# Optimization experiments

Measured on AMD Instinct MI355X. Metric: run time of the kernel, lower is better.

The kernel has to match this reference:

```python
import jax, jax.numpy as jnp
import numpy as np


def setup_inputs() -> dict:
    key = jax.random.key(0)
    # D must equal N for the elementwise Multiply([inputs, attn]) to broadcast.
    B, N = 16, 1024
    x = jax.random.normal(key, (B, N, N), dtype=jnp.float32)
    return {"x": x}


def reference(x) -> jnp.ndarray:
    # scores[b,i,j] = <x[b,i,:], x[b,j,:]>  -> [B, N, N]
    scores = jnp.einsum("bid,bjd->bij", x, x)
    attn = jax.nn.softmax(scores, axis=-1)
    # NOTE: elementwise multiply (not a weighted sum) — faithful to the source.
    return x * attn
```

## Files before the change

kernel.cpp:

```cpp
#include <hip/hip_runtime.h>
#include <hip/hip_bf16.h>

#define BATCH   16
#define NN      1024
#define ROWS    64
#define NWAVES  8
#define NTHR    512
#define KSTEP   32
#define NCT     8
#define MT      4

typedef __attribute__((ext_vector_type(8))) short short8;
typedef __attribute__((ext_vector_type(4))) float f32x4;

static __device__ __forceinline__ unsigned short cvt_bf16(float f) {
    unsigned int u = __builtin_bit_cast(unsigned int, f);
    u += 0x7fffu + ((u >> 16) & 1u);
    return (unsigned short)(u >> 16);
}

static __device__ __forceinline__ short8 cvt8(float4 u0, float4 u1) {
    short8 r;
    r[0] = (short)cvt_bf16(u0.x); r[1] = (short)cvt_bf16(u0.y);
    r[2] = (short)cvt_bf16(u0.z); r[3] = (short)cvt_bf16(u0.w);
    r[4] = (short)cvt_bf16(u1.x); r[5] = (short)cvt_bf16(u1.y);
    r[6] = (short)cvt_bf16(u1.z); r[7] = (short)cvt_bf16(u1.w);
    return r;
}

__global__ __launch_bounds__(256)
void cvt_kernel(const float* __restrict__ x, unsigned short* __restrict__ xw) {
    const int n4 = BATCH * NN * NN / 4;
    int i = blockIdx.x * 256 + threadIdx.x;
    const int stride = gridDim.x * 256;
    for (; i < n4; i += stride) {
        float4 v = reinterpret_cast<const float4*>(x)[i];
        ushort4 h;
        h.x = cvt_bf16(v.x); h.y = cvt_bf16(v.y);
        h.z = cvt_bf16(v.z); h.w = cvt_bf16(v.w);
        reinterpret_cast<ushort4*>(xw)[i] = h;
    }
}

template<int BF16WS>
__global__ __launch_bounds__(NTHR, 2)
void attn_fused(const float* __restrict__ x, const unsigned short* __restrict__ xw,
                float* __restrict__ out) {
    const int wg   = blockIdx.x;
    const int t    = wg >> 3;
    const int b    = (wg & 7) + 8 * (t >> 4);
    const int i0   = (t & 15) * ROWS;
    const int tid  = threadIdx.x;
    const int lane = tid & 63;
    const int wid  = tid >> 6;
    const int l15  = lane & 15;
    const int g    = lane >> 4;

    const float* xb = x + (size_t)b * NN * NN;

    __shared__ unsigned short ldsA[ROWS * NN];
    __shared__ float redbuf[NWAVES][ROWS];

    if (BF16WS) {
        const unsigned short* Aw = xw + (size_t)b * NN * NN + (size_t)i0 * NN;
        #pragma unroll
        for (int it = 0; it < (ROWS * NN / 4) / NTHR; ++it) {
            int f4  = tid + it * NTHR;
            int row = f4 >> 8;
            int d   = (f4 & 255) << 2;
            ushort4 h = *reinterpret_cast<const ushort4*>(Aw + row * NN + d);
            int e = (row * NN + d) ^ ((row & 15) << 3);
            *reinterpret_cast<ushort4*>(&ldsA[e]) = h;
        }
    } else {
        const float* Ar = xb + (size_t)i0 * NN;
        #pragma unroll
        for (int it = 0; it < (ROWS * NN / 4) / NTHR; ++it) {
            int f4  = tid + it * NTHR;
            int row = f4 >> 8;
            int d   = (f4 & 255) << 2;
            float4 v = *reinterpret_cast<const float4*>(Ar + row * NN + d);
            int e = (row * NN + d) ^ ((row & 15) << 3);
            ushort4 h;
            h.x = cvt_bf16(v.x); h.y = cvt_bf16(v.y);
            h.z = cvt_bf16(v.z); h.w = cvt_bf16(v.w);
            *reinterpret_cast<ushort4*>(&ldsA[e]) = h;
        }
    }
    __syncthreads();

    f32x4 acc[MT][NCT];
    #pragma unroll
    for (int r = 0; r < MT; ++r)
        #pragma unroll
        for (int ct = 0; ct < NCT; ++ct)
            acc[r][ct] = (f32x4){0.f, 0.f, 0.f, 0.f};

    const int jb = wid * (NCT * 16);

    if (BF16WS) {
        const unsigned short* Bb = xw + (size_t)b * NN * NN
                                      + (size_t)(jb + l15) * NN + g * 8;
        #pragma unroll 1
        for (int k = 0; k < NN; k += KSTEP) {
            short8 ar[MT];
            #pragma unroll
            for (int r = 0; r < MT; ++r) {
                int e = ((r * 16 + l15) * NN + k + g * 8) ^ (l15 << 3);
                ar[r] = *reinterpret_cast<const short8*>(&ldsA[e]);
            }
            #pragma unroll
            for (int ct = 0; ct < NCT; ++ct) {
                short8 bf = *reinterpret_cast<const short8*>(Bb + ct * (16 * NN) + k);
                #pragma unroll
                for (int r = 0; r < MT; ++r)
                    acc[r][ct] = __builtin_amdgcn_mfma_f32_16x16x32_bf16(
                        ar[r], bf, acc[r][ct], 0, 0, 0);
            }
        }
    } else {
        const float* Bb = xb + (size_t)(jb + l15) * NN + g * 8;
        #pragma unroll 1
        for (int k = 0; k < NN; k += KSTEP) {
            short8 ar[MT];
            #pragma unroll
            for (int r = 0; r < MT; ++r) {
                int e = ((r * 16 + l15) * NN + k + g * 8) ^ (l15 << 3);
                ar[r] = *reinterpret_cast<const short8*>(&ldsA[e]);
            }
            #pragma unroll
            for (int ct = 0; ct < NCT; ++ct) {
                const float* p = Bb + ct * (16 * NN) + k;
                float4 u0 = *reinterpret_cast<const float4*>(p);
                float4 u1 = *reinterpret_cast<const float4*>(p + 4);
                short8 bf = cvt8(u0, u1);
                #pragma unroll
                for (int r = 0; r < MT; ++r)
                    acc[r][ct] = __builtin_amdgcn_mfma_f32_16x16x32_bf16(
                        ar[r], bf, acc[r][ct], 0, 0, 0);
            }
        }
    }

    float mrow[MT][4];
    #pragma unroll
    for (int r = 0; r < MT; ++r)
        #pragma unroll
        for (int q = 0; q < 4; ++q) {
            float m = acc[r][0][q];
            #pragma unroll
            for (int ct = 1; ct < NCT; ++ct) m = fmaxf(m, acc[r][ct][q]);
            #pragma unroll
            for (int s = 1; s < 16; s <<= 1) m = fmaxf(m, __shfl_xor(m, s, 64));
            mrow[r][q] = m;
        }
    if (l15 == 0) {
        #pragma unroll
        for (int r = 0; r < MT; ++r)
            #pragma unroll
            for (int q = 0; q < 4; ++q)
                redbuf[wid][r * 16 + g * 4 + q] = mrow[r][q];
    }
    __syncthreads();
    #pragma unroll
    for (int r = 0; r < MT; ++r)
        #pragma unroll
        for (int q = 0; q < 4; ++q) {
            int row = r * 16 + g * 4 + q;
            float m = redbuf[0][row];
            #pragma unroll
            for (int w = 1; w < NWAVES; ++w) m = fmaxf(m, redbuf[w][row]);
            mrow[r][q] = m;
        }
    __syncthreads();

    float srow[MT][4];
    #pragma unroll
    for (int r = 0; r < MT; ++r)
        #pragma unroll
        for (int q = 0; q < 4; ++q) {
            float s = 0.f;
            #pragma unroll
            for (int ct = 0; ct < NCT; ++ct) {
                float e = __expf(acc[r][ct][q] - mrow[r][q]);
                acc[r][ct][q] = e;
                s += e;
            }
            #pragma unroll
            for (int sh = 1; sh < 16; sh <<= 1) s += __shfl_xor(s, sh, 64);
            srow[r][q] = s;
        }
    if (l15 == 0) {
        #pragma unroll
        for (int r = 0; r < MT; ++r)
            #pragma unroll
            for (int q = 0; q < 4; ++q)
                redbuf[wid][r * 16 + g * 4 + q] = srow[r][q];
    }
    __syncthreads();

    float* ob = out + (size_t)b * NN * NN;
    #pragma unroll
    for (int r = 0; r < MT; ++r)
        #pragma unroll
        for (int q = 0; q < 4; ++q) {
            int row = r * 16 + g * 4 + q;
            float tot = redbuf[0][row];
            #pragma unroll
            for (int w = 1; w < NWAVES; ++w) tot += redbuf[w][row];
            float inv = 1.0f / tot;
            const size_t rowoff = (size_t)(i0 + row) * NN;
            #pragma unroll
            for (int ct = 0; ct < NCT; ++ct) {
                int j_ = jb + ct * 16 + l15;
                ob[rowoff + j_] = xb[rowoff + j_] * acc[r][ct][q] * inv;
            }
        }
}

extern "C" void kernel_launch(void* const* d_in, const int* in_sizes, int n_in,
                              void* d_out, int out_size, void* d_ws, size_t ws_size,
                              hipStream_t stream) {
    const float* x = (const float*)d_in[0];
    float* out = (float*)d_out;
    const size_t need = (size_t)BATCH * NN * NN * sizeof(unsigned short);
    dim3 grid(BATCH * (NN / ROWS));
    if (ws_size >= need) {
        unsigned short* xw = (unsigned short*)d_ws;
        cvt_kernel<<<2048, 256, 0, stream>>>(x, xw);
        attn_fused<1><<<grid, NTHR, 0, stream>>>(x, xw, out);
    } else {
        attn_fused<0><<<grid, NTHR, 0, stream>>>(x, nullptr, out);
    }
}
```

Before: 190.7 us.

## Use 16-wave workgroups with 64-deep K steps and MFMA priority boost

The workspace path now launches 1024-thread workgroups of 16 waves, each wave covering 4 column tiles instead of 8. This halves the accumulator register footprint per wave and doubles the waves sharing the LDS-resident A tile. The K loop now advances by 64, loading two B fragments per column tile up front and wrapping the MFMA block in s_setprio to favour the matrix issue. The fallback path is split into its own kernel with the old parameters. With the 128KB LDS tile, only one workgroup fits per CU, so occupancy relies entirely on the 16 waves within it.

After: 192.5 us. No clear change (+0.9%).

```diff
diff --git a/kernel.cpp b/kernel.cpp
--- a/kernel.cpp
+++ b/kernel.cpp
@@ -4,10 +4,9 @@
 #define BATCH   16
 #define NN      1024
 #define ROWS    64
-#define NWAVES  8
-#define NTHR    512
-#define KSTEP   32
-#define NCT     8
+#define NWAVES  16
+#define NTHR    1024
+#define NCT     4
 #define MT      4
 
 typedef __attribute__((ext_vector_type(8))) short short8;
@@ -17,15 +16,6 @@
     unsigned int u = __builtin_bit_cast(unsigned int, f);
     u += 0x7fffu + ((u >> 16) & 1u);
     return (unsigned short)(u >> 16);
-}
-
-static __device__ __forceinline__ short8 cvt8(float4 u0, float4 u1) {
-    short8 r;
-    r[0] = (short)cvt_bf16(u0.x); r[1] = (short)cvt_bf16(u0.y);
-    r[2] = (short)cvt_bf16(u0.z); r[3] = (short)cvt_bf16(u0.w);
-    r[4] = (short)cvt_bf16(u1.x); r[5] = (short)cvt_bf16(u1.y);
-    r[6] = (short)cvt_bf16(u1.z); r[7] = (short)cvt_bf16(u1.w);
-    return r;
 }
 
 __global__ __launch_bounds__(256)
@@ -42,10 +32,9 @@
     }
 }
 
-template<int BF16WS>
-__global__ __launch_bounds__(NTHR, 2)
-void attn_fused(const float* __restrict__ x, const unsigned short* __restrict__ xw,
-                float* __restrict__ out) {
+__global__ __launch_bounds__(NTHR)
+void attn_v3(const float* __restrict__ x, const unsigned short* __restrict__ xw,
+             float* __restrict__ out) {
     const int wg   = blockIdx.x;
     const int t    = wg >> 3;
     const int b    = (wg & 7) + 8 * (t >> 4);
@@ -61,7 +50,7 @@
     __shared__ unsigned short ldsA[ROWS * NN];
     __shared__ float redbuf[NWAVES][ROWS];
 
-    if (BF16WS) {
+    {
         const unsigned short* Aw = xw + (size_t)b * NN * NN + (size_t)i0 * NN;
         #pragma unroll
         for (int it = 0; it < (ROWS * NN / 4) / NTHR; ++it) {
@@ -72,11 +61,158 @@
             int e = (row * NN + d) ^ ((row & 15) << 3);
             *reinterpret_cast<ushort4*>(&ldsA[e]) = h;
         }
-    } else {
+    }
+    __syncthreads();
+
+    f32x4 acc[MT][NCT];
+    #pragma unroll
+    for (int r = 0; r < MT; ++r)
+        #pragma unroll
+        for (int ct = 0; ct < NCT; ++ct)
+            acc[r][ct] = (f32x4){0.f, 0.f, 0.f, 0.f};
+
+    const int jb = wid * (NCT * 16);
+    const unsigned short* Bb = xw + (size_t)b * NN * NN
+                                  + (size_t)(jb + l15) * NN + g * 8;
+
+    #pragma unroll 1
+    for (int k = 0; k < NN; k += 64) {
+        short8 blo[NCT], bhi[NCT];
+        #pragma unroll
+        for (int ct = 0; ct < NCT; ++ct) {
+            const unsigned short* p = Bb + ct * (16 * NN) + k;
+            blo[ct] = *reinterpret_cast<const short8*>(p);
+            bhi[ct] = *reinterpret_cast<const short8*>(p + 32);
+        }
+        __builtin_amdgcn_s_setprio(1);
+        #pragma unroll
+        for (int r = 0; r < MT; ++r) {
+            const int base = (r * 16 + l15) * NN + g * 8;
+            short8 a0 = *reinterpret_cast<const short8*>(
+                            &ldsA[(base + k)      ^ (l15 << 3)]);
+            short8 a1 = *reinterpret_cast<const short8*>(
+                            &ldsA[(base + k + 32) ^ (l15 << 3)]);
+            #pragma unroll
+            for (int ct = 0; ct < NCT; ++ct) {
+                acc[r][ct] = __builtin_amdgcn_mfma_f32_16x16x32_bf16(
+                    a0, blo[ct], acc[r][ct], 0, 0, 0);
+                acc[r][ct] = __builtin_amdgcn_mfma_f32_16x16x32_bf16(
+                    a1, bhi[ct], acc[r][ct], 0, 0, 0);
+            }
+        }
+        __builtin_amdgcn_s_setprio(0);
+    }
+
+    float mrow[MT][4];
+    #pragma unroll
+    for (int r = 0; r < MT; ++r)
+        #pragma unroll
+        for (int q = 0; q < 4; ++q) {
+            float m = acc[r][0][q];
+            #pragma unroll
+            for (int ct = 1; ct < NCT; ++ct) m = fmaxf(m, acc[r][ct][q]);
+            #pragma unroll
+            for (int s = 1; s < 16; s <<= 1) m = fmaxf(m, __shfl_xor(m, s, 64));
+            mrow[r][q] = m;
+        }
+    if (l15 == 0) {
+        #pragma unroll
+        for (int r = 0; r < MT; ++r)
+            #pragma unroll
+            for (int q = 0; q < 4; ++q)
+                redbuf[wid][r * 16 + g * 4 + q] = mrow[r][q];
+    }
+    __syncthreads();
+    #pragma unroll
+    for (int r = 0; r < MT; ++r)
+        #pragma unroll
+        for (int q = 0; q < 4; ++q) {
+            int row = r * 16 + g * 4 + q;
+            float m = redbuf[0][row];
+            #pragma unroll
+            for (int w = 1; w < NWAVES; ++w) m = fmaxf(m, redbuf[w][row]);
+            mrow[r][q] = m;
+        }
+    __syncthreads();
+
+    float srow[MT][4];
+    #pragma unroll
+    for (int r = 0; r < MT; ++r)
+        #pragma unroll
+        for (int q = 0; q < 4; ++q) {
+            float s = 0.f;
+            #pragma unroll
+            for (int ct = 0; ct < NCT; ++ct) {
+                float e = __expf(acc[r][ct][q] - mrow[r][q]);
+                acc[r][ct][q] = e;
+                s += e;
+            }
+            #pragma unroll
+            for (int sh = 1; sh < 16; sh <<= 1) s += __shfl_xor(s, sh, 64);
+            srow[r][q] = s;
+        }
+    if (l15 == 0) {
+        #pragma unroll
+        for (int r = 0; r < MT; ++r)
+            #pragma unroll
+            for (int q = 0; q < 4; ++q)
+                redbuf[wid][r * 16 + g * 4 + q] = srow[r][q];
+    }
+    __syncthreads();
+
+    float* ob = out + (size_t)b * NN * NN;
+    #pragma unroll
+    for (int r = 0; r < MT; ++r)
+        #pragma unroll
+        for (int q = 0; q < 4; ++q) {
+            int row = r * 16 + g * 4 + q;
+            float tot = redbuf[0][row];
+            #pragma unroll
+            for (int w = 1; w < NWAVES; ++w) tot += redbuf[w][row];
+            float inv = 1.0f / tot;
+            const size_t rowoff = (size_t)(i0 + row) * NN;
+            #pragma unroll
+            for (int ct = 0; ct < NCT; ++ct) {
+                int j_ = jb + ct * 16 + l15;
+                ob[rowoff + j_] = xb[rowoff + j_] * acc[r][ct][q] * inv;
+            }
+        }
+}
+
+#define FB_NWAVES 8
+#define FB_NTHR   512
+#define FB_NCT    8
+
+static __device__ __forceinline__ short8 cvt8(float4 u0, float4 u1) {
+    short8 r;
+    r[0] = (short)cvt_bf16(u0.x); r[1] = (short)cvt_bf16(u0.y);
+    r[2] = (short)cvt_bf16(u0.z); r[3] = (short)cvt_bf16(u0.w);
+    r[4] = (short)cvt_bf16(u1.x); r[5] = (short)cvt_bf16(u1.y);
+    r[6] = (short)cvt_bf16(u1.z); r[7] = (short)cvt_bf16(u1.w);
+    return r;
+}
+
+__global__ __launch_bounds__(FB_NTHR, 2)
+void attn_fb(const float* __restrict__ x, float* __restrict__ out) {
+    const int wg   = blockIdx.x;
+    const int t    = wg >> 3;
+    const int b    = (wg & 7) + 8 * (t >> 4);
+    const int i0   = (t & 15) * ROWS;
+    const int tid  = threadIdx.x;
+    const int lane = tid & 63;
+    const int wid  = tid >> 6;
+    const int l15  = lane & 15;
+    const int g    = lane >> 4;
+
+    const float* xb = x + (size_t)b * NN * NN;
+    __shared__ unsigned short ldsA[ROWS * NN];
+    __shared__ float redbuf[FB_NWAVES][ROWS];
+
+    {
         const float* Ar = xb + (size_t)i0 * NN;
         #pragma unroll
-        for (int it = 0; it < (ROWS * NN / 4) / NTHR; ++it) {
-            int f4  = tid + it * NTHR;
+        for (int it = 0; it < (ROWS * NN / 4) / FB_NTHR; ++it) {
+            int f4  = tid + it * FB_NTHR;
             int row = f4 >> 8;
             int d   = (f4 & 255) << 2;
             float4 v = *reinterpret_cast<const float4*>(Ar + row * NN + d);
@@ -89,56 +225,34 @@
     }
     __syncthreads();
 
-    f32x4 acc[MT][NCT];
-    #pragma unroll
-    for (int r = 0; r < MT; ++r)
-        #pragma unroll
-        for (int ct = 0; ct < NCT; ++ct)
+    f32x4 acc[MT][FB_NCT];
+    #pragma unroll
+    for (int r = 0; r < MT; ++r)
+        #pragma unroll
+        for (int ct = 0; ct < FB_NCT; ++ct)
             acc[r][ct] = (f32x4){0.f, 0.f, 0.f, 0.f};
 
-    const int jb = wid * (NCT * 16);
-
-    if (BF16WS) {
-        const unsigned short* Bb = xw + (size_t)b * NN * NN
-                                      + (size_t)(jb + l15) * NN + g * 8;
-        #pragma unroll 1
-        for (int k = 0; k < NN; k += KSTEP) {
-            short8 ar[MT];
-            #pragma unroll
-            for (int r = 0; r < MT; ++r) {
-                int e = ((r * 16 + l15) * NN + k + g * 8) ^ (l15 << 3);
-                ar[r] = *reinterpret_cast<const short8*>(&ldsA[e]);
-            }
-            #pragma unroll
-            for (int ct = 0; ct < NCT; ++ct) {
-                short8 bf = *reinterpret_cast<const short8*>(Bb + ct * (16 * NN) + k);
-                #pragma unroll
-                for (int r = 0; r < MT; ++r)
-                    acc[r][ct] = __builtin_amdgcn_mfma_f32_16x16x32_bf16(
-                        ar[r], bf, acc[r][ct], 0, 0, 0);
-            }
-        }
-    } else {
-        const float* Bb = xb + (size_t)(jb + l15) * NN + g * 8;
-        #pragma unroll 1
-        for (int k = 0; k < NN; k += KSTEP) {
-            short8 ar[MT];
-            #pragma unroll
-            for (int r = 0; r < MT; ++r) {
-                int e = ((r * 16 + l15) * NN + k + g * 8) ^ (l15 << 3);
-                ar[r] = *reinterpret_cast<const short8*>(&ldsA[e]);
-            }
-            #pragma unroll
-            for (int ct = 0; ct < NCT; ++ct) {
-                const float* p = Bb + ct * (16 * NN) + k;
-                float4 u0 = *reinterpret_cast<const float4*>(p);
-                float4 u1 = *reinterpret_cast<const float4*>(p + 4);
-                short8 bf = cvt8(u0, u1);
-                #pragma unroll
-                for (int r = 0; r < MT; ++r)
-                    acc[r][ct] = __builtin_amdgcn_mfma_f32_16x16x32_bf16(
-                        ar[r], bf, acc[r][ct], 0, 0, 0);
-            }
+    const int jb = wid * (FB_NCT * 16);
+    const float* Bb = xb + (size_t)(jb + l15) * NN + g * 8;
+
+    #pragma unroll 1
+    for (int k = 0; k < NN; k += 32) {
+        short8 ar[MT];
+        #pragma unroll
+        for (int r = 0; r < MT; ++r) {
+            int e = ((r * 16 + l15) * NN + k + g * 8) ^ (l15 << 3);
+            ar[r] = *reinterpret_cast<const short8*>(&ldsA[e]);
+        }
+        #pragma unroll
+        for (int ct = 0; ct < FB_NCT; ++ct) {
+            const float* p = Bb + ct * (16 * NN) + k;
+            float4 u0 = *reinterpret_cast<const float4*>(p);
+            float4 u1 = *reinterpret_cast<const float4*>(p + 4);
+            short8 bf = cvt8(u0, u1);
+            #pragma unroll
+            for (int r = 0; r < MT; ++r)
+                acc[r][ct] = __builtin_amdgcn_mfma_f32_16x16x32_bf16(
+                    ar[r], bf, acc[r][ct], 0, 0, 0);
         }
     }
 
@@ -149,7 +263,7 @@
         for (int q = 0; q < 4; ++q) {
             float m = acc[r][0][q];
             #pragma unroll
-            for (int ct = 1; ct < NCT; ++ct) m = fmaxf(m, acc[r][ct][q]);
+            for (int ct = 1; ct < FB_NCT; ++ct) m = fmaxf(m, acc[r][ct][q]);
             #pragma unroll
             for (int s = 1; s < 16; s <<= 1) m = fmaxf(m, __shfl_xor(m, s, 64));
             mrow[r][q] = m;
@@ -169,7 +283,7 @@
             int row = r * 16 + g * 4 + q;
             float m = redbuf[0][row];
             #pragma unroll
-            for (int w = 1; w < NWAVES; ++w) m = fmaxf(m, redbuf[w][row]);
+            for (int w = 1; w < FB_NWAVES; ++w) m = fmaxf(m, redbuf[w][row]);
             mrow[r][q] = m;
         }
     __syncthreads();
@@ -181,7 +295,7 @@
         for (int q = 0; q < 4; ++q) {
             float s = 0.f;
             #pragma unroll
-            for (int ct = 0; ct < NCT; ++ct) {
+            for (int ct = 0; ct < FB_NCT; ++ct) {
                 float e = __expf(acc[r][ct][q] - mrow[r][q]);
                 acc[r][ct][q] = e;
                 s += e;
@@ -207,11 +321,11 @@
             int row = r * 16 + g * 4 + q;
             float tot = redbuf[0][row];
             #pragma unroll
-            for (int w = 1; w < NWAVES; ++w) tot += redbuf[w][row];
+            for (int w = 1; w < FB_NWAVES; ++w) tot += redbuf[w][row];
             float inv = 1.0f / tot;
             const size_t rowoff = (size_t)(i0 + row) * NN;
             #pragma unroll
-            for (int ct = 0; ct < NCT; ++ct) {
+            for (int ct = 0; ct < FB_NCT; ++ct) {
                 int j_ = jb + ct * 16 + l15;
                 ob[rowoff + j_] = xb[rowoff + j_] * acc[r][ct][q] * inv;
             }
@@ -228,8 +342,8 @@
     if (ws_size >= need) {
         unsigned short* xw = (unsigned short*)d_ws;
         cvt_kernel<<<2048, 256, 0, stream>>>(x, xw);
-        attn_fused<1><<<grid, NTHR, 0, stream>>>(x, xw, out);
+        attn_v3<<<grid, NTHR, 0, stream>>>(x, xw, out);
     } else {
-        attn_fused<0><<<grid, NTHR, 0, stream>>>(x, nullptr, out);
-    }
-}
+        attn_fb<<<grid, FB_NTHR, 0, stream>>>(x, out);
+    }
+}
```
